# Kernel tuning notes

Measured on AMD Instinct MI355X. Metric: run time of the kernel, lower is better.

The kernel has to match this reference:

```python
import jax, jax.numpy as jnp
import numpy as np

BETA = 0.25

def setup_inputs() -> dict:
    key = jax.random.key(0)
    k1, k2 = jax.random.split(key)
    N, K, D = 262144, 256, 256
    z_e = jax.random.normal(k1, (N, D), dtype=jnp.float32)
    # nn.Embedding init: uniform(-1/K, 1/K)
    emb_weight = jax.random.uniform(k2, (K, D), dtype=jnp.float32, minval=-1.0 / K, maxval=1.0 / K)
    return {"z_e": z_e, "emb_weight": emb_weight}

def reference(z_e, emb_weight):
    # squared L2 distances: ||z||^2 + ||e||^2 - 2 z e^T  -> [N, K]
    dist = (jnp.sum(z_e ** 2, axis=1, keepdims=True)
            + jnp.sum(emb_weight ** 2, axis=1)
            - 2.0 * jnp.matmul(z_e, emb_weight.T))
    encoding_inds = jnp.argmin(dist, axis=1)  # [N]
    z_q = emb_weight[encoding_inds]           # [N, D]

    sg = jax.lax.stop_gradient
    commitment_loss = jnp.mean((sg(z_e) - z_q) ** 2)
    codebook_loss = jnp.mean((z_e - sg(z_q)) ** 2)
    loss = codebook_loss + BETA * commitment_loss

    # straight-through estimator
    z_q_st = z_e + sg(z_q - z_e)
    return z_q_st, encoding_inds, loss
```

## Files before the change

kernel.cpp:

```cpp
#include <hip/hip_runtime.h>

typedef __attribute__((ext_vector_type(8))) short bf16x8;
typedef __attribute__((ext_vector_type(4))) float f32x4;
typedef __attribute__((ext_vector_type(4))) unsigned short us4;
typedef __attribute__((ext_vector_type(8))) unsigned short us8;

#define NROWS 262144
#define KC 256
#define DD 256
#define BM 128
#define DK 32
#define TAU 1.5e-3f
#define FCAP 65536

__device__ __forceinline__ float np_pw128_sq(const float* a) {
    float r[8];
#pragma unroll
    for (int j = 0; j < 8; ++j) r[j] = __fmul_rn(a[j], a[j]);
    for (int i = 8; i < 128; i += 8) {
#pragma unroll
        for (int j = 0; j < 8; ++j)
            r[j] = __fadd_rn(r[j], __fmul_rn(a[i + j], a[i + j]));
    }
    float t01 = __fadd_rn(r[0], r[1]), t23 = __fadd_rn(r[2], r[3]);
    float t45 = __fadd_rn(r[4], r[5]), t67 = __fadd_rn(r[6], r[7]);
    return __fadd_rn(__fadd_rn(t01, t23), __fadd_rn(t45, t67));
}
__device__ __forceinline__ float np_sum256_sq(const float* a) {
    return __fadd_rn(np_pw128_sq(a), np_pw128_sq(a + 128));
}

__device__ __forceinline__ unsigned short bf16_rne(float x) {
    unsigned b = __float_as_uint(x);
    b += 0x7FFFu + ((b >> 16) & 1u);
    return (unsigned short)(b >> 16);
}

__global__ void vq_prep(const float* __restrict__ emb, float* __restrict__ se,
                        double* __restrict__ accum, int* __restrict__ gcnt) {
    int k = threadIdx.x;
    if (k == 0) { *accum = 0.0; *gcnt = 0; }
    se[k] = np_sum256_sq(emb + (size_t)k * DD);
}

__global__ void vq_split(const float* __restrict__ emb, unsigned short* __restrict__ ph) {
    int f = (blockIdx.x * 256 + threadIdx.x) * 4;
    float4 v = *reinterpret_cast<const float4*>(emb + f);
    int k = f >> 8, d = f & 255;
    int off = (d >> 5) * (KC * DK) + k * DK + (d & 31);
    us4 h;
    h[0] = bf16_rne(v.x); h[1] = bf16_rne(v.y);
    h[2] = bf16_rne(v.z); h[3] = bf16_rne(v.w);
    *reinterpret_cast<us4*>(ph + off) = h;
}

__global__ __launch_bounds__(256, 2)
void vq_main(const float* __restrict__ ze, const unsigned short* __restrict__ ph,
             const float* __restrict__ se_g, float* __restrict__ out_inds,
             double* __restrict__ accum, int* __restrict__ glist, int* __restrict__ gcnt)
{
    __shared__ float se_s[KC];
    __shared__ float wv1[4 * BM], wv2[4 * BM];
    __shared__ int   wk1[4 * BM];
    __shared__ float red[256];

    const int t = threadIdx.x;
    const int w = t >> 6;
    const int q = (t >> 4) & 3;
    const int c = t & 15;
    const size_t m0 = (size_t)blockIdx.x * BM;

    se_s[t] = se_g[t];

    bf16x8 bfr[4][8];
#pragma unroll
    for (int nf = 0; nf < 4; ++nf)
#pragma unroll
        for (int dci = 0; dci < 8; ++dci)
            bfr[nf][dci] = *reinterpret_cast<const bf16x8*>(
                ph + dci * (KC * DK) + (w * 64 + nf * 16 + c) * DK + q * 8);

    __syncthreads();

    float se_v[4];
#pragma unroll
    for (int nf = 0; nf < 4; ++nf) se_v[nf] = se_s[64 * w + 16 * nf + c];

    float sz_run = 0.f;

    float4 z0[8], z1[8];
    {
        const float* zb = ze + (m0 + c) * DD + q * 8;
#pragma unroll
        for (int dci = 0; dci < 8; ++dci) {
            z0[dci] = *reinterpret_cast<const float4*>(zb + dci * 32);
            z1[dci] = *reinterpret_cast<const float4*>(zb + dci * 32 + 4);
        }
    }

    for (int step = 0; step < BM / 16; ++step) {
        bf16x8 afrag[8];
#pragma unroll
        for (int dci = 0; dci < 8; ++dci) {
            float4 a = z0[dci], b = z1[dci];
            if (w == 0) {
                sz_run = fmaf(a.x, a.x, sz_run); sz_run = fmaf(a.y, a.y, sz_run);
                sz_run = fmaf(a.z, a.z, sz_run); sz_run = fmaf(a.w, a.w, sz_run);
                sz_run = fmaf(b.x, b.x, sz_run); sz_run = fmaf(b.y, b.y, sz_run);
                sz_run = fmaf(b.z, b.z, sz_run); sz_run = fmaf(b.w, b.w, sz_run);
            }
            us8 h;
            h[0] = bf16_rne(a.x); h[1] = bf16_rne(a.y); h[2] = bf16_rne(a.z); h[3] = bf16_rne(a.w);
            h[4] = bf16_rne(b.x); h[5] = bf16_rne(b.y); h[6] = bf16_rne(b.z); h[7] = bf16_rne(b.w);
            afrag[dci] = __builtin_bit_cast(bf16x8, h);
        }
        if (step < BM / 16 - 1) {
            const float* zb = ze + (m0 + (step + 1) * 16 + c) * DD + q * 8;
#pragma unroll
            for (int dci = 0; dci < 8; ++dci) {
                z0[dci] = *reinterpret_cast<const float4*>(zb + dci * 32);
                z1[dci] = *reinterpret_cast<const float4*>(zb + dci * 32 + 4);
            }
        }
        f32x4 acc[4];
#pragma unroll
        for (int nf = 0; nf < 4; ++nf) acc[nf] = (f32x4){0.f, 0.f, 0.f, 0.f};
#pragma unroll
        for (int dci = 0; dci < 8; ++dci)
#pragma unroll
            for (int nf = 0; nf < 4; ++nf)
                acc[nf] = __builtin_amdgcn_mfma_f32_16x16x32_bf16(afrag[dci], bfr[nf][dci], acc[nf], 0, 0, 0);

#pragma unroll
        for (int j = 0; j < 4; ++j) {
            float v1 = 3.4e38f, v2 = 3.4e38f; int k1 = 0x7fffffff;
#pragma unroll
            for (int nf = 0; nf < 4; ++nf) {
                int k = 64 * w + 16 * nf + c;
                float dv = fmaf(-2.f, acc[nf][j], se_v[nf]);
                if (dv < v1) { v2 = v1; v1 = dv; k1 = k; }
                else if (dv < v2) { v2 = dv; }
            }
#pragma unroll
            for (int off = 1; off < 16; off <<= 1) {
                float ov1 = __shfl_xor(v1, off, 64);
                float ov2 = __shfl_xor(v2, off, 64);
                int   ok1 = __shfl_xor(k1, off, 64);
                bool other = (ov1 < v1) || (ov1 == v1 && ok1 < k1);
                float nv2 = other ? fminf(v1, ov2) : fminf(v2, ov1);
                if (other) { v1 = ov1; k1 = ok1; }
                v2 = nv2;
            }
            if (c == 0) {
                int row = step * 16 + 4 * q + j;
                wv1[w * BM + row] = v1;
                wv2[w * BM + row] = v2;
                wk1[w * BM + row] = k1;
            }
        }
    }
    __syncthreads();

    float lossv = 0.f;
    if (t < BM) {
        float v1 = wv1[t], v2 = wv2[t]; int k1 = wk1[t];
#pragma unroll
        for (int ww = 1; ww < 4; ++ww) {
            float ov1 = wv1[ww * BM + t], ov2 = wv2[ww * BM + t];
            int ok1 = wk1[ww * BM + t];
            bool other = (ov1 < v1) || (ov1 == v1 && ok1 < k1);
            float nv2 = other ? fminf(v1, ov2) : fminf(v2, ov1);
            if (other) { v1 = ov1; k1 = ok1; }
            v2 = nv2;
        }
        out_inds[m0 + t] = (float)k1;
        lossv = v1;
        if (v2 - v1 < TAU) {
            int s_ = atomicAdd(gcnt, 1);
            if (s_ < FCAP) glist[s_] = (int)(m0 + t);
        }
    }
    __syncthreads();

    red[t] = (w == 0 ? sz_run : 0.f) + (t < BM ? lossv : 0.f);
    __syncthreads();
    for (int s = 128; s > 0; s >>= 1) {
        if (t < s) red[t] += red[t + s];
        __syncthreads();
    }
    if (t == 0) atomicAdd(accum, (double)red[0]);
}

__global__ __launch_bounds__(256)
void vq_fix(const float* __restrict__ ze, const float* __restrict__ emb,
            const float* __restrict__ se_g, const int* __restrict__ glist,
            const int* __restrict__ gcnt, float* __restrict__ out_inds)
{
    __shared__ float dq[16][256];
    __shared__ float srow_s[16];
    __shared__ int   rowid_s[16];

    const int t = threadIdx.x;
    int F = *gcnt; if (F > FCAP) F = FCAP;
    const float se_k = se_g[t];
    const float4* e4p = reinterpret_cast<const float4*>(emb + (size_t)t * DD);

    for (int g = blockIdx.x * 16; g < F; g += gridDim.x * 16) {
        __syncthreads();
        if (t < 16) {
            int idx = g + t; if (idx > F - 1) idx = F - 1;
            int row = glist[idx];
            rowid_s[t] = row;
            srow_s[t] = np_sum256_sq(ze + (size_t)row * DD);
        }
        __syncthreads();

        const float* zp[16];
#pragma unroll
        for (int r = 0; r < 16; ++r)
            zp[r] = ze + (size_t)__builtin_amdgcn_readfirstlane(rowid_s[r]) * DD;

        float m32[16];
#pragma unroll
        for (int r = 0; r < 16; ++r) m32[r] = 0.f;
        for (int d4 = 0; d4 < 64; ++d4) {
            float4 e4 = e4p[d4];
            const int d = d4 * 4;
#pragma unroll
            for (int r = 0; r < 16; ++r) {
                m32[r] = __fmaf_rn(zp[r][d + 0], e4.x, m32[r]);
                m32[r] = __fmaf_rn(zp[r][d + 1], e4.y, m32[r]);
                m32[r] = __fmaf_rn(zp[r][d + 2], e4.z, m32[r]);
                m32[r] = __fmaf_rn(zp[r][d + 3], e4.w, m32[r]);
            }
        }
#pragma unroll
        for (int r = 0; r < 16; ++r) {
            float A = __fadd_rn(srow_s[r], se_k);
            dq[r][t] = __fsub_rn(A, __fmul_rn(2.0f, m32[r]));
        }
        __syncthreads();

        {
            const int r = t >> 4, p = t & 15;
            float bv = 3.4e38f; int bk = 0x7fffffff;
#pragma unroll
            for (int i = 0; i < 16; ++i) {
                int k = p * 16 + i;
                float v = dq[r][k];
                if (v < bv) { bv = v; bk = k; }
            }
#pragma unroll
            for (int off = 1; off < 16; off <<= 1) {
                float ov = __shfl_xor(bv, off, 64);
                int   ok = __shfl_xor(bk, off, 64);
                if (ov < bv || (ov == bv && ok < bk)) { bv = ov; bk = ok; }
            }
            if (p == 0 && g + r < F) out_inds[rowid_s[r]] = (float)bk;
        }
        __syncthreads();
    }
}

__global__ __launch_bounds__(256)
void vq_gather(const float* __restrict__ emb, const float* __restrict__ out_inds,
               float* __restrict__ out_zq)
{
    const int t = threadIdx.x;
    const int w = t >> 6, l = t & 63;
    const size_t m0 = (size_t)blockIdx.x * 128 + (size_t)w * 32;
#pragma unroll 8
    for (int r = 0; r < 32; ++r) {
        int k = (int)out_inds[m0 + r];
        float4 v = *reinterpret_cast<const float4*>(emb + (size_t)k * DD + l * 4);
        *reinterpret_cast<float4*>(out_zq + (m0 + r) * DD + l * 4) = v;
    }
}

__global__ void vq_fin(const double* __restrict__ accum, float* __restrict__ out_loss) {
    *out_loss = (float)(1.25 * (*accum) / ((double)NROWS * (double)DD));
}

extern "C" void kernel_launch(void* const* d_in, const int* in_sizes, int n_in,
                              void* d_out, int out_size, void* d_ws, size_t ws_size,
                              hipStream_t stream) {
    const float* ze  = (const float*)d_in[0];
    const float* emb = (const float*)d_in[1];
    float* out      = (float*)d_out;
    float* out_zq   = out;
    float* out_inds = out + (size_t)NROWS * DD;
    float* out_loss = out + (size_t)NROWS * DD + NROWS;

    double* accum = (double*)d_ws;
    int*    gcnt  = (int*)((char*)d_ws + 8);
    float*  se    = (float*)((char*)d_ws + 256);
    int*    glist = (int*)((char*)d_ws + 4096);
    unsigned short* ph = (unsigned short*)((char*)d_ws + 4096 + 262144);

    vq_prep<<<1, 256, 0, stream>>>(emb, se, accum, gcnt);
    vq_split<<<KC * DD / (256 * 4), 256, 0, stream>>>(emb, ph);
    vq_main<<<NROWS / BM, 256, 0, stream>>>(ze, ph, se, out_inds, accum, glist, gcnt);
    vq_fix<<<1024, 256, 0, stream>>>(ze, emb, se, glist, gcnt, out_inds);
    vq_gather<<<NROWS / 128, 256, 0, stream>>>(emb, out_inds, out_zq);
    vq_fin<<<1, 1, 0, stream>>>(accum, out_loss);
}
```

Before: 383.2 us.

## Stage z tile and codebook slices in LDS with double-buffered K-slab pipeline

The main kernel no longer keeps the whole bf16 codebook in registers with per-step z loads. It now loads a 64-row z tile once, converts it to bf16 into padded LDS, and streams 32-wide codebook slabs through a double-buffered LDS buffer. Each wave computes a 4x4 grid of MFMA tiles and the split kernel writes a fragment-friendly codebook layout. This cuts register pressure and changes data reuse. In exchange it adds about 50KB of LDS per block and a barrier per slab, which may limit occupancy.

```diff
diff --git a/kernel.cpp b/kernel.cpp
--- a/kernel.cpp
+++ b/kernel.cpp
@@ -8,10 +8,10 @@
 #define NROWS 262144
 #define KC 256
 #define DD 256
-#define BM 128
-#define DK 32
+#define BM 64
 #define TAU 1.5e-3f
 #define FCAP 65536
+#define ZSW 264
 
 __device__ __forceinline__ float np_pw128_sq(const float* a) {
     float r[8];
@@ -47,7 +47,7 @@
     int f = (blockIdx.x * 256 + threadIdx.x) * 4;
     float4 v = *reinterpret_cast<const float4*>(emb + f);
     int k = f >> 8, d = f & 255;
-    int off = (d >> 5) * (KC * DK) + k * DK + (d & 31);
+    int off = (d >> 5) * 8192 + (k >> 4) * 512 + (k & 15) * 32 + ((d >> 3) & 3) * 8 + (d & 7);
     us4 h;
     h[0] = bf16_rne(v.x); h[1] = bf16_rne(v.y);
     h[2] = bf16_rne(v.z); h[3] = bf16_rne(v.w);
@@ -59,6 +59,8 @@
              const float* __restrict__ se_g, float* __restrict__ out_inds,
              double* __restrict__ accum, int* __restrict__ glist, int* __restrict__ gcnt)
 {
+    __shared__ __attribute__((aligned(16))) unsigned short zl[BM * ZSW];
+    __shared__ __attribute__((aligned(16))) unsigned short eb[2][8192];
     __shared__ float se_s[KC];
     __shared__ float wv1[4 * BM], wv2[4 * BM];
     __shared__ int   wk1[4 * BM];
@@ -72,72 +74,79 @@
 
     se_s[t] = se_g[t];
 
-    bf16x8 bfr[4][8];
-#pragma unroll
-    for (int nf = 0; nf < 4; ++nf)
-#pragma unroll
-        for (int dci = 0; dci < 8; ++dci)
-            bfr[nf][dci] = *reinterpret_cast<const bf16x8*>(
-                ph + dci * (KC * DK) + (w * 64 + nf * 16 + c) * DK + q * 8);
-
+    float4 zr[16];
+#pragma unroll
+    for (int it = 0; it < 16; ++it) {
+        int idx = it * 256 + t;
+        int row = idx >> 6, c4 = idx & 63;
+        zr[it] = *reinterpret_cast<const float4*>(ze + (m0 + row) * DD + c4 * 4);
+    }
+    float sz_acc = 0.f;
+#pragma unroll
+    for (int it = 0; it < 16; ++it) {
+        float4 v = zr[it];
+        int idx = it * 256 + t;
+        int row = idx >> 6, c4 = idx & 63;
+        sz_acc = fmaf(v.x, v.x, sz_acc); sz_acc = fmaf(v.y, v.y, sz_acc);
+        sz_acc = fmaf(v.z, v.z, sz_acc); sz_acc = fmaf(v.w, v.w, sz_acc);
+        us4 h;
+        h[0] = bf16_rne(v.x); h[1] = bf16_rne(v.y);
+        h[2] = bf16_rne(v.z); h[3] = bf16_rne(v.w);
+        *reinterpret_cast<us4*>(&zl[row * ZSW + c4 * 4]) = h;
+    }
+
+    us8 er[4];
+#pragma unroll
+    for (int i = 0; i < 4; ++i)
+        er[i] = *reinterpret_cast<const us8*>(ph + (i * 256 + t) * 8);
+#pragma unroll
+    for (int i = 0; i < 4; ++i)
+        *reinterpret_cast<us8*>(&eb[0][(i * 256 + t) * 8]) = er[i];
     __syncthreads();
 
-    float se_v[4];
-#pragma unroll
-    for (int nf = 0; nf < 4; ++nf) se_v[nf] = se_s[64 * w + 16 * nf + c];
-
-    float sz_run = 0.f;
-
-    float4 z0[8], z1[8];
-    {
-        const float* zb = ze + (m0 + c) * DD + q * 8;
-#pragma unroll
-        for (int dci = 0; dci < 8; ++dci) {
-            z0[dci] = *reinterpret_cast<const float4*>(zb + dci * 32);
-            z1[dci] = *reinterpret_cast<const float4*>(zb + dci * 32 + 4);
-        }
-    }
-
-    for (int step = 0; step < BM / 16; ++step) {
-        bf16x8 afrag[8];
-#pragma unroll
-        for (int dci = 0; dci < 8; ++dci) {
-            float4 a = z0[dci], b = z1[dci];
-            if (w == 0) {
-                sz_run = fmaf(a.x, a.x, sz_run); sz_run = fmaf(a.y, a.y, sz_run);
-                sz_run = fmaf(a.z, a.z, sz_run); sz_run = fmaf(a.w, a.w, sz_run);
-                sz_run = fmaf(b.x, b.x, sz_run); sz_run = fmaf(b.y, b.y, sz_run);
-                sz_run = fmaf(b.z, b.z, sz_run); sz_run = fmaf(b.w, b.w, sz_run);
-            }
-            us8 h;
-            h[0] = bf16_rne(a.x); h[1] = bf16_rne(a.y); h[2] = bf16_rne(a.z); h[3] = bf16_rne(a.w);
-            h[4] = bf16_rne(b.x); h[5] = bf16_rne(b.y); h[6] = bf16_rne(b.z); h[7] = bf16_rne(b.w);
-            afrag[dci] = __builtin_bit_cast(bf16x8, h);
-        }
-        if (step < BM / 16 - 1) {
-            const float* zb = ze + (m0 + (step + 1) * 16 + c) * DD + q * 8;
-#pragma unroll
-            for (int dci = 0; dci < 8; ++dci) {
-                z0[dci] = *reinterpret_cast<const float4*>(zb + dci * 32);
-                z1[dci] = *reinterpret_cast<const float4*>(zb + dci * 32 + 4);
-            }
-        }
-        f32x4 acc[4];
-#pragma unroll
-        for (int nf = 0; nf < 4; ++nf) acc[nf] = (f32x4){0.f, 0.f, 0.f, 0.f};
-#pragma unroll
-        for (int dci = 0; dci < 8; ++dci)
-#pragma unroll
-            for (int nf = 0; nf < 4; ++nf)
-                acc[nf] = __builtin_amdgcn_mfma_f32_16x16x32_bf16(afrag[dci], bfr[nf][dci], acc[nf], 0, 0, 0);
-
+    f32x4 acc[4][4];
+#pragma unroll
+    for (int i = 0; i < 4; ++i)
+#pragma unroll
+        for (int j = 0; j < 4; ++j) acc[i][j] = (f32x4){0.f, 0.f, 0.f, 0.f};
+
+#pragma unroll
+    for (int dci = 0; dci < 8; ++dci) {
+        const int cur = dci & 1;
+        if (dci < 7) {
+            const unsigned short* src = ph + (dci + 1) * 8192;
+#pragma unroll
+            for (int i = 0; i < 4; ++i)
+                er[i] = *reinterpret_cast<const us8*>(src + (i * 256 + t) * 8);
+        }
+        bf16x8 af[4];
+#pragma unroll
+        for (int mf = 0; mf < 4; ++mf)
+            af[mf] = *reinterpret_cast<const bf16x8*>(&zl[(16 * mf + c) * ZSW + dci * 32 + q * 8]);
+#pragma unroll
+        for (int nf = 0; nf < 4; ++nf) {
+            bf16x8 bf = *reinterpret_cast<const bf16x8*>(&eb[cur][((4 * w + nf) * 64 + c * 4 + q) * 8]);
+#pragma unroll
+            for (int mf = 0; mf < 4; ++mf)
+                acc[mf][nf] = __builtin_amdgcn_mfma_f32_16x16x32_bf16(af[mf], bf, acc[mf][nf], 0, 0, 0);
+        }
+        if (dci < 7) {
+#pragma unroll
+            for (int i = 0; i < 4; ++i)
+                *reinterpret_cast<us8*>(&eb[cur ^ 1][(i * 256 + t) * 8]) = er[i];
+        }
+        __syncthreads();
+    }
+
+#pragma unroll
+    for (int mf = 0; mf < 4; ++mf)
 #pragma unroll
         for (int j = 0; j < 4; ++j) {
             float v1 = 3.4e38f, v2 = 3.4e38f; int k1 = 0x7fffffff;
 #pragma unroll
             for (int nf = 0; nf < 4; ++nf) {
                 int k = 64 * w + 16 * nf + c;
-                float dv = fmaf(-2.f, acc[nf][j], se_v[nf]);
+                float dv = fmaf(-2.f, acc[mf][nf][j], se_s[k]);
                 if (dv < v1) { v2 = v1; v1 = dv; k1 = k; }
                 else if (dv < v2) { v2 = dv; }
             }
@@ -152,13 +161,10 @@
                 v2 = nv2;
             }
             if (c == 0) {
-                int row = step * 16 + 4 * q + j;
-                wv1[w * BM + row] = v1;
-                wv2[w * BM + row] = v2;
-                wk1[w * BM + row] = k1;
-            }
-        }
-    }
+                int row = 16 * mf + 4 * q + j;
+                wv1[w * BM + row] = v1; wv2[w * BM + row] = v2; wk1[w * BM + row] = k1;
+            }
+        }
     __syncthreads();
 
     float lossv = 0.f;
@@ -182,7 +188,7 @@
     }
     __syncthreads();
 
-    red[t] = (w == 0 ? sz_run : 0.f) + (t < BM ? lossv : 0.f);
+    red[t] = sz_acc + (t < BM ? lossv : 0.f);
     __syncthreads();
     for (int s = 128; s > 0; s >>= 1) {
         if (t < s) red[t] += red[t + s];
```

Result: faster. 322.9 us (-15.7%).
